# Kernel tuning notes

Measured on AMD Instinct MI355X. Metric: run time of the kernel, lower is better.

Reference implementation:

```python
import jax, jax.numpy as jnp
import numpy as np

DIM = 384
NH = 12
HEAD = DIM // NH
WS = (7, 7, 7)
L = WS[0] * WS[1] * WS[2]          # 343 tokens per window
NW = 64                             # number of windows (mask.shape[0])
B = 1                               # batch per window group
N = B * NW                          # leading dim of x
TBL = (2 * WS[0] - 1) * (2 * WS[1] - 1) * (2 * WS[2] - 1)  # 2197
SCALE = HEAD ** -0.5


def _rel_index():
    # Standard Swin 3D relative position index, shape (L, L), values in [0, TBL)
    coords = np.stack(np.meshgrid(*[np.arange(w) for w in WS], indexing='ij')).reshape(3, -1)  # (3, L)
    rel = coords[:, :, None] - coords[:, None, :]                     # (3, L, L)
    rel = rel + (np.array(WS) - 1)[:, None, None]                     # shift to >= 0
    s1 = (2 * WS[1] - 1) * (2 * WS[2] - 1)
    s2 = (2 * WS[2] - 1)
    idx = rel[0] * s1 + rel[1] * s2 + rel[2]
    return jnp.asarray(idx, jnp.int32)


def setup_inputs() -> dict:
    key = jax.random.key(0)
    k_x, k_m, k_qkv, k_tbl, k_pw = jax.random.split(key, 5)
    x = jax.random.normal(k_x, (N, L, DIM), dtype=jnp.float32)
    mask = jax.random.bernoulli(k_m, 0.5, (NW, L, L))                 # bool, True = masked
    qkv_w = jax.random.normal(k_qkv, (DIM, 3 * DIM), dtype=jnp.float32) * 0.02
    table = jax.random.normal(k_tbl, (TBL, NH), dtype=jnp.float32) * 0.02
    proj_w = jax.random.normal(k_pw, (DIM, DIM), dtype=jnp.float32) * 0.02
    proj_b = jnp.zeros((DIM,), dtype=jnp.float32)
    rel_idx = _rel_index()
    return {"x": x, "qkv_w": qkv_w, "table": table, "proj_w": proj_w,
            "proj_b": proj_b, "mask": mask, "rel_idx": rel_idx}


def reference(x, qkv_w, table, proj_w, proj_b, mask, rel_idx):
    n, l, _ = x.shape
    # QKV projection (no bias, qkv_bias=False)
    qkv = (x @ qkv_w).reshape(n, l, 3, NH, HEAD).transpose(2, 0, 3, 1, 4)  # (3, n, nh, l, ch)
    q, k, v = qkv[0], qkv[1], qkv[2]
    attn = jnp.einsum('nhlc,nhmc->nhlm', q * SCALE, k)                 # (n, nh, l, l)
    # gather relative position bias: (L*L, nh) -> (nh, L, L)
    bias = table[rel_idx.reshape(-1)].reshape(l, l, NH).transpose(2, 0, 1)
    attn = attn + bias[None]
    # per-window boolean mask: attn viewed as (batch, nw, nh, l, l)
    attn = attn.reshape(-1, NW, NH, l, l)
    attn = jnp.where(mask[None, :, None], -jnp.inf, attn).reshape(n, NH, l, l)
    attn = jax.nn.softmax(attn, axis=-1)
    out = jnp.einsum('nhlm,nhmc->nhlc', attn, v)                       # (n, nh, l, ch)
    out = out.transpose(0, 2, 1, 3).reshape(n, l, DIM)
    return out @ proj_w + proj_b
```

## Files before the change

### kernel.cpp

```cpp
#include <hip/hip_runtime.h>


#define DIMD 384
#define NHH 12
#define HEADD 32
#define LL 343
#define NWW 64
#define NTOK (NWW * LL)
#define MPT 176
#define MP (MPT * 128)
#define LP 352
#define QT 22
#define KS 40
#define VTS 360
#define PSB 40
#define MW 12
#define CSS 136
#define SCALE_ 0.17677669529663687f
#define LOG2E_ 1.4426950408889634f
#define NEGBIG_ (-1.0e4f)

typedef _Float16 f16;
typedef _Float16 v8h __attribute__((ext_vector_type(8)));
typedef _Float16 v4h __attribute__((ext_vector_type(4)));
typedef float v4f __attribute__((ext_vector_type(4)));

__device__ __forceinline__ void async_cp16(const void* g, void* l) {
    __builtin_amdgcn_global_load_lds(
        (const __attribute__((address_space(1))) void*)g,
        (__attribute__((address_space(3))) void*)l, 16, 0, 0);
}

constexpr size_t HBUF = (size_t)NHH * MP * HEADD * 2;
constexpr size_t OFF_Q    = 0;
constexpr size_t OFF_K    = OFF_Q  + HBUF;
constexpr size_t OFF_V    = OFF_K  + HBUF;
constexpr size_t OFF_AO   = OFF_V  + HBUF;
constexpr size_t OFF_BT   = OFF_AO + (size_t)MP * DIMD * 2;
constexpr size_t OFF_WT   = OFF_BT + (size_t)NHH * LP * LP * 4;
constexpr size_t OFF_PWT  = OFF_WT + (size_t)3 * DIMD * DIMD * 2;
constexpr size_t OFF_MTB  = OFF_PWT + (size_t)DIMD * DIMD * 2;

constexpr int SMEM_ATTN = LP * KS * 2 + 32 * VTS * 2 + LP * MW * 4 + 8 * 16 * PSB * 2;

#define S0 (NTOK * DIMD / 4)
#define S1 (3 * DIMD * DIMD)
#define S2 (DIMD * DIMD)
#define S3 (NHH * LP * LP)
#define S4 (NWW * MW * LP)
#define SPREP (S0 + S1 + S2 + S3 + S4)

__global__ __launch_bounds__(256) void prep_all(
    const float* __restrict__ x, f16* __restrict__ xh,
    const float* __restrict__ qkv_w, f16* __restrict__ wt,
    const float* __restrict__ proj_w, f16* __restrict__ pwt,
    const float* __restrict__ table, const int* __restrict__ rel, float* __restrict__ btf,
    const int* __restrict__ mask, unsigned int* __restrict__ mtb) {
    int t = blockIdx.x * 256 + threadIdx.x;
    if (t < S0) {
        float4 v = *(const float4*)(x + (size_t)t * 4);
        v4h o; o[0] = (f16)v.x; o[1] = (f16)v.y; o[2] = (f16)v.z; o[3] = (f16)v.w;
        *(v4h*)(xh + (size_t)t * 4) = o;
    } else if (t < S0 + S1) {
        int e = t - S0;
        int n = e / DIMD, k = e % DIMD;
        wt[e] = (f16)qkv_w[(size_t)k * (3 * DIMD) + n];
    } else if (t < S0 + S1 + S2) {
        int e = t - S0 - S1;
        int n = e / DIMD, k = e % DIMD;
        pwt[e] = (f16)proj_w[(size_t)k * DIMD + n];
    } else if (t < S0 + S1 + S2 + S3) {
        int e = t - S0 - S1 - S2;
        int h = e / (LP * LP), rem = e % (LP * LP);
        int rq = rem / (LP * 4);
        int rem2 = rem % (LP * 4);
        int col = rem2 >> 2, e2 = rem2 & 3;
        int r = rq * 4 + e2;
        float v = NEGBIG_;
        if (col < LL && r < LL) v = table[(size_t)rel[r * LL + col] * NHH + h] * LOG2E_;
        btf[e] = v;
    } else if (t < SPREP) {
        int e = t - S0 - S1 - S2 - S3;
        int n = e / (MW * LP), rem = e % (MW * LP);
        int wg = rem / LP, col = rem % LP;
        unsigned int wd = 0;
        if (col < LL) {
            int rbase = wg * 32;
#pragma unroll 4
            for (int b = 0; b < 32; ++b) {
                int r = rbase + b;
                if (r < LL && mask[((size_t)n * LL + r) * LL + col]) wd |= (1u << b);
            }
        }
        mtb[((size_t)n * LP + col) * MW + wg] = wd;
    }
}

__global__ __launch_bounds__(256) void qkv_gemm(
    const f16* __restrict__ xh, const f16* __restrict__ wt,
    f16* __restrict__ qb, f16* __restrict__ kb, f16* __restrict__ vb) {
    __shared__ f16 ABs[8192];
    f16* As = ABs;
    f16* Bs = ABs + 4096;
    const int lin = blockIdx.x;
    const int m0 = ((lin / 72) * 8 + (lin & 7)) * 128;
    const int n0 = ((lin >> 3) % 9) * 128;
    const int tid = threadIdx.x;
    const int wave = tid >> 6, lane = tid & 63;
    const int quad = lane >> 4, l15 = lane & 15;
    const int wm = (wave >> 1) * 64, wn = (wave & 1) * 64;
    const int srow = (lane >> 2);
    const int scol = (lane & 3) * 8;
    const f16* ga0 = xh + (size_t)(m0 + wave * 32 + srow) * DIMD + scol;
    const f16* ga1 = xh + (size_t)(m0 + wave * 32 + 16 + srow) * DIMD + scol;
    const f16* gb0 = wt + (size_t)(n0 + wave * 32 + srow) * DIMD + scol;
    const f16* gb1 = wt + (size_t)(n0 + wave * 32 + 16 + srow) * DIMD + scol;
    f16* la0 = As + (wave * 2) * 512;
    f16* la1 = As + (wave * 2 + 1) * 512;
    f16* lb0 = Bs + (wave * 2) * 512;
    f16* lb1 = Bs + (wave * 2 + 1) * 512;
    v4f acc[4][4] = {};
    for (int k0 = 0; k0 < DIMD; k0 += 32) {
        async_cp16(ga0 + k0, la0);
        async_cp16(ga1 + k0, la1);
        async_cp16(gb0 + k0, lb0);
        async_cp16(gb1 + k0, lb1);
        __syncthreads();
        v8h a[4], b[4];
#pragma unroll
        for (int i = 0; i < 4; ++i) a[i] = *(const v8h*)(As + (wm + i * 16 + l15) * 32 + quad * 8);
#pragma unroll
        for (int j = 0; j < 4; ++j) b[j] = *(const v8h*)(Bs + (wn + j * 16 + l15) * 32 + quad * 8);
#pragma unroll
        for (int i = 0; i < 4; ++i)
#pragma unroll
            for (int j = 0; j < 4; ++j)
                acc[i][j] = __builtin_amdgcn_mfma_f32_16x16x32_f16(a[i], b[j], acc[i][j], 0, 0, 0);
        __syncthreads();
    }
    const int t = n0 / DIMD;
    f16* dst = (t == 0) ? qb : (t == 1) ? kb : vb;
    const float sc = (t == 0) ? (SCALE_ * LOG2E_) : 1.0f;
    const int nrel = n0 - t * DIMD;
    f16* Cs = ABs;
    const int rl0 = (wave >> 1) * 16 + quad * 4;
#pragma unroll
    for (int i = 0; i < 4; ++i) {
#pragma unroll
        for (int e = 0; e < 4; ++e)
#pragma unroll
            for (int j = 0; j < 4; ++j)
                Cs[(rl0 + e) * CSS + wn + j * 16 + l15] = (f16)(acc[i][j][e] * sc);
        __syncthreads();
#pragma unroll
        for (int c = 0; c < 2; ++c) {
            int idx = c * 256 + tid;
            int rl = idx >> 4, col8 = (idx & 15) * 8;
            int gm = m0 + ((rl < 16) ? (i * 16 + rl) : (48 + i * 16 + rl));
            if (gm < NTOK) {
                int col = nrel + col8;
                size_t off = (size_t)(col >> 5) * ((size_t)MP * HEADD)
                           + (col & 31) + (size_t)gm * HEADD;
                *(v8h*)(dst + off) = *(const v8h*)(Cs + rl * CSS + col8);
            }
        }
        __syncthreads();
    }
}

__global__ __launch_bounds__(512, 4) void attn_kernel(
    const f16* __restrict__ qb, const f16* __restrict__ kb, const f16* __restrict__ vb,
    const float* __restrict__ biasT, const unsigned int* __restrict__ mtb,
    f16* __restrict__ ao) {
    extern __shared__ char smem[];
    f16* Ks  = (f16*)smem;
    f16* Vts = Ks + LP * KS;
    unsigned int* mtbL = (unsigned int*)(Vts + 32 * VTS);
    f16* Ps  = (f16*)(mtbL + LP * MW);
    const int n = blockIdx.x, h = blockIdx.y;
    const int tid = threadIdx.x, wave = tid >> 6, lane = tid & 63;
    const int quad = lane >> 4, l15 = lane & 15;
    const size_t slice = ((size_t)h * MP + n * LL) * HEADD;
    const f16* qg = qb + slice;
    const f16* kg = kb + slice;
    const f16* vg = vb + slice;
    for (int i = tid; i < LL * 8; i += 512) {
        int row = i >> 3, c4 = i & 7;
        *(ushort4*)(Ks + row * KS + c4 * 4) = *(const ushort4*)(kg + i * 4);
    }
    for (int i = tid; i < (LP - LL) * 8; i += 512) {
        int row = LL + (i >> 3), c4 = i & 7;
        *(ushort4*)(Ks + row * KS + c4 * 4) = make_ushort4(0, 0, 0, 0);
    }
    for (int i = tid; i < LL * 8; i += 512) {
        int key = i >> 3, c4 = (i & 7) * 4;
        ushort4 vv = *(const ushort4*)(vg + key * HEADD + c4);
        f16* d = Vts + c4 * VTS + key;
        d[0] = *(const f16*)&vv.x; d[VTS] = *(const f16*)&vv.y;
        d[2 * VTS] = *(const f16*)&vv.z; d[3 * VTS] = *(const f16*)&vv.w;
    }
    for (int i = tid; i < 32 * (LP - LL); i += 512) {
        int ch = i / (LP - LL), key = LL + i % (LP - LL);
        Vts[ch * VTS + key] = (f16)0.f;
    }
    {
        const unsigned int* mg = mtb + (size_t)n * LP * MW;
        for (int i = tid; i < LP * MW; i += 512) mtbL[i] = mg[i];
    }
    __syncthreads();
    f16* Pw = Ps + wave * (16 * PSB);
    const float* bth = biasT + (size_t)h * LP * LP;
    const v8h ones = {(f16)1.f, (f16)1.f, (f16)1.f, (f16)1.f,
                      (f16)1.f, (f16)1.f, (f16)1.f, (f16)1.f};
    for (int qt = wave; qt < QT; qt += 8) {
        v8h af = *(const v8h*)(qg + (qt * 16 + l15) * HEADD + quad * 8);
        const int r0 = qt * 16 + quad * 4;
        const int rword = r0 >> 5, rsh = r0 & 31;
        const float* bq = bth + (size_t)(qt * 4 + quad) * (LP * 4);
        v4f o0 = {}, o1 = {}, o2 = {};
        v4f cinN[2];
        cinN[0] = *(const v4f*)(bq + (size_t)l15 * 4);
        cinN[1] = *(const v4f*)(bq + (size_t)(16 + l15) * 4);
#pragma unroll
        for (int ktp = 0; ktp < 11; ++ktp) {
            v4f cin[2] = {cinN[0], cinN[1]};
            if (ktp < 10) {
                cinN[0] = *(const v4f*)(bq + (size_t)((ktp * 2 + 2) * 16 + l15) * 4);
                cinN[1] = *(const v4f*)(bq + (size_t)((ktp * 2 + 3) * 16 + l15) * 4);
            }
            unsigned int mw[2]; v8h bf[2]; v4f s[2];
#pragma unroll
            for (int half = 0; half < 2; ++half) {
                const int col = (ktp * 2 + half) * 16 + l15;
                mw[half] = mtbL[col * MW + rword];
                bf[half] = *(const v8h*)(Ks + col * KS + quad * 8);
            }
#pragma unroll
            for (int half = 0; half < 2; ++half) {
                v4f c = cin[half];
#pragma unroll
                for (int e = 0; e < 4; ++e)
                    if ((mw[half] >> (rsh + e)) & 1u) c[e] = NEGBIG_;
                s[half] = __builtin_amdgcn_mfma_f32_16x16x32_f16(af, bf[half], c, 0, 0, 0);
            }
#pragma unroll
            for (int half = 0; half < 2; ++half)
#pragma unroll
                for (int e = 0; e < 4; ++e) {
                    float p = __builtin_amdgcn_exp2f(s[half][e]);
                    Pw[(quad * 4 + e) * PSB + half * 16 + l15] = (f16)p;
                }
            v8h a  = *(const v8h*)(Pw + l15 * PSB + quad * 8);
            v8h b0 = *(const v8h*)(Vts + l15 * VTS + ktp * 32 + quad * 8);
            v8h b1 = *(const v8h*)(Vts + (16 + l15) * VTS + ktp * 32 + quad * 8);
            o0 = __builtin_amdgcn_mfma_f32_16x16x32_f16(a, b0, o0, 0, 0, 0);
            o1 = __builtin_amdgcn_mfma_f32_16x16x32_f16(a, b1, o1, 0, 0, 0);
            o2 = __builtin_amdgcn_mfma_f32_16x16x32_f16(a, ones, o2, 0, 0, 0);
        }
#pragma unroll
        for (int e = 0; e < 4; ++e) {
            int r = r0 + e;
            if (r < LL) {
                float inv = 1.f / o2[e];
                f16* orow = ao + ((size_t)(n * LL + r)) * DIMD + h * HEADD;
                orow[l15] = (f16)(o0[e] * inv);
                orow[16 + l15] = (f16)(o1[e] * inv);
            }
        }
    }
}

__global__ __launch_bounds__(256) void proj_gemm(
    const f16* __restrict__ ao, const f16* __restrict__ pwt,
    const float* __restrict__ pb, float* __restrict__ out) {
    __shared__ f16 As[128 * 32];
    __shared__ f16 Bs[128 * 32];
    const int lin = blockIdx.x;
    const int m0 = ((lin / 24) * 8 + (lin & 7)) * 128;
    const int n0 = ((lin >> 3) % 3) * 128;
    const int tid = threadIdx.x;
    const int wave = tid >> 6, lane = tid & 63;
    const int quad = lane >> 4, l15 = lane & 15;
    const int wm = (wave >> 1) * 64, wn = (wave & 1) * 64;
    const int srow = (lane >> 2);
    const int scol = (lane & 3) * 8;
    const f16* ga0 = ao + (size_t)(m0 + wave * 32 + srow) * DIMD + scol;
    const f16* ga1 = ao + (size_t)(m0 + wave * 32 + 16 + srow) * DIMD + scol;
    const f16* gb0 = pwt + (size_t)(n0 + wave * 32 + srow) * DIMD + scol;
    const f16* gb1 = pwt + (size_t)(n0 + wave * 32 + 16 + srow) * DIMD + scol;
    f16* la0 = As + (wave * 2) * 512;
    f16* la1 = As + (wave * 2 + 1) * 512;
    f16* lb0 = Bs + (wave * 2) * 512;
    f16* lb1 = Bs + (wave * 2 + 1) * 512;
    v4f acc[4][4] = {};
    for (int k0 = 0; k0 < DIMD; k0 += 32) {
        async_cp16(ga0 + k0, la0);
        async_cp16(ga1 + k0, la1);
        async_cp16(gb0 + k0, lb0);
        async_cp16(gb1 + k0, lb1);
        __syncthreads();
        v8h a[4], b[4];
#pragma unroll
        for (int i = 0; i < 4; ++i) a[i] = *(const v8h*)(As + (wm + i * 16 + l15) * 32 + quad * 8);
#pragma unroll
        for (int j = 0; j < 4; ++j) b[j] = *(const v8h*)(Bs + (wn + j * 16 + l15) * 32 + quad * 8);
#pragma unroll
        for (int i = 0; i < 4; ++i)
#pragma unroll
            for (int j = 0; j < 4; ++j)
                acc[i][j] = __builtin_amdgcn_mfma_f32_16x16x32_f16(a[i], b[j], acc[i][j], 0, 0, 0);
        __syncthreads();
    }
#pragma unroll
    for (int i = 0; i < 4; ++i)
#pragma unroll
        for (int e = 0; e < 4; ++e) {
            int gm = m0 + wm + i * 16 + quad * 4 + e;
            if (gm < NTOK) {
#pragma unroll
                for (int j = 0; j < 4; ++j) {
                    int gn = n0 + wn + j * 16 + l15;
                    out[(size_t)gm * DIMD + gn] = acc[i][j][e] + pb[gn];
                }
            }
        }
}

extern "C" void kernel_launch(void* const* d_in, const int* in_sizes, int n_in,
                              void* d_out, int out_size, void* d_ws, size_t ws_size,
                              hipStream_t stream) {
    const float* x      = (const float*)d_in[0];
    const float* qkv_w  = (const float*)d_in[1];
    const float* table  = (const float*)d_in[2];
    const float* proj_w = (const float*)d_in[3];
    const float* proj_b = (const float*)d_in[4];
    const int* mask     = (const int*)d_in[5];
    const int* rel      = (const int*)d_in[6];
    float* out = (float*)d_out;
    char* ws = (char*)d_ws;

    f16* q    = (f16*)(ws + OFF_Q);
    f16* k    = (f16*)(ws + OFF_K);
    f16* v    = (f16*)(ws + OFF_V);
    f16* xh   = (f16*)(ws + OFF_AO);
    f16* ao   = (f16*)(ws + OFF_AO);
    float* bt = (float*)(ws + OFF_BT);
    f16* wt   = (f16*)(ws + OFF_WT);
    f16* pwt  = (f16*)(ws + OFF_PWT);
    unsigned int* mtb = (unsigned int*)(ws + OFF_MTB);

    hipFuncSetAttribute((const void*)attn_kernel,
                        hipFuncAttributeMaxDynamicSharedMemorySize, SMEM_ATTN);

    prep_all<<<(SPREP + 255) / 256, 256, 0, stream>>>(
        x, xh, qkv_w, wt, proj_w, pwt, table, rel, bt, mask, mtb);
    qkv_gemm<<<dim3(MPT * 9), 256, 0, stream>>>(xh, wt, q, k, v);
    attn_kernel<<<dim3(NWW, NHH), 512, SMEM_ATTN, stream>>>(q, k, v, bt, mtb, ao);
    proj_gemm<<<dim3(MPT * 3), 256, 0, stream>>>(ao, pwt, proj_b, out);
}
```

Before: 227.0 us.

## Shrink attention LDS: reuse K padding for P staging, read mask from global

The attention kernel drops its separate LDS buffers for the mask bits and the per-wave P tile. P is now staged in the unused padding columns (32..39) of the K rows, and mask words are prefetched from global memory into registers alongside the bias. Blocks shrink from 512 to 256 threads (4 waves, each handling more query tiles) to cut LDS use and allow more resident blocks per CU. The risks are extra global/L2 traffic for the mask and less parallelism per block, while the layout of P in the K padding looks likely to cause LDS bank conflicts.

```diff
diff --git a/kernel.cpp b/kernel.cpp
--- a/kernel.cpp
+++ b/kernel.cpp
@@ -13,7 +13,6 @@
 #define QT 22
 #define KS 40
 #define VTS 360
-#define PSB 40
 #define MW 12
 #define CSS 136
 #define SCALE_ 0.17677669529663687f
@@ -41,7 +40,7 @@
 constexpr size_t OFF_PWT  = OFF_WT + (size_t)3 * DIMD * DIMD * 2;
 constexpr size_t OFF_MTB  = OFF_PWT + (size_t)DIMD * DIMD * 2;
 
-constexpr int SMEM_ATTN = LP * KS * 2 + 32 * VTS * 2 + LP * MW * 4 + 8 * 16 * PSB * 2;
+constexpr int SMEM_ATTN = LP * KS * 2 + 32 * VTS * 2;
 
 #define S0 (NTOK * DIMD / 4)
 #define S1 (3 * DIMD * DIMD)
@@ -168,15 +167,13 @@
     }
 }
 
-__global__ __launch_bounds__(512, 4) void attn_kernel(
+__global__ __launch_bounds__(256, 3) void attn_kernel(
     const f16* __restrict__ qb, const f16* __restrict__ kb, const f16* __restrict__ vb,
     const float* __restrict__ biasT, const unsigned int* __restrict__ mtb,
     f16* __restrict__ ao) {
     extern __shared__ char smem[];
     f16* Ks  = (f16*)smem;
     f16* Vts = Ks + LP * KS;
-    unsigned int* mtbL = (unsigned int*)(Vts + 32 * VTS);
-    f16* Ps  = (f16*)(mtbL + LP * MW);
     const int n = blockIdx.x, h = blockIdx.y;
     const int tid = threadIdx.x, wave = tid >> 6, lane = tid & 63;
     const int quad = lane >> 4, l15 = lane & 15;
@@ -184,57 +181,57 @@
     const f16* qg = qb + slice;
     const f16* kg = kb + slice;
     const f16* vg = vb + slice;
-    for (int i = tid; i < LL * 8; i += 512) {
+    for (int i = tid; i < LL * 8; i += 256) {
         int row = i >> 3, c4 = i & 7;
         *(ushort4*)(Ks + row * KS + c4 * 4) = *(const ushort4*)(kg + i * 4);
     }
-    for (int i = tid; i < (LP - LL) * 8; i += 512) {
+    for (int i = tid; i < (LP - LL) * 8; i += 256) {
         int row = LL + (i >> 3), c4 = i & 7;
         *(ushort4*)(Ks + row * KS + c4 * 4) = make_ushort4(0, 0, 0, 0);
     }
-    for (int i = tid; i < LL * 8; i += 512) {
+    for (int i = tid; i < LL * 8; i += 256) {
         int key = i >> 3, c4 = (i & 7) * 4;
         ushort4 vv = *(const ushort4*)(vg + key * HEADD + c4);
         f16* d = Vts + c4 * VTS + key;
         d[0] = *(const f16*)&vv.x; d[VTS] = *(const f16*)&vv.y;
         d[2 * VTS] = *(const f16*)&vv.z; d[3 * VTS] = *(const f16*)&vv.w;
     }
-    for (int i = tid; i < 32 * (LP - LL); i += 512) {
+    for (int i = tid; i < 32 * (LP - LL); i += 256) {
         int ch = i / (LP - LL), key = LL + i % (LP - LL);
         Vts[ch * VTS + key] = (f16)0.f;
     }
-    {
-        const unsigned int* mg = mtb + (size_t)n * LP * MW;
-        for (int i = tid; i < LP * MW; i += 512) mtbL[i] = mg[i];
-    }
     __syncthreads();
-    f16* Pw = Ps + wave * (16 * PSB);
+    f16* Pbase = Ks + (size_t)(wave * 64) * KS + 32;
+    const unsigned int* mwin = mtb + (size_t)n * LP * MW;
     const float* bth = biasT + (size_t)h * LP * LP;
     const v8h ones = {(f16)1.f, (f16)1.f, (f16)1.f, (f16)1.f,
                       (f16)1.f, (f16)1.f, (f16)1.f, (f16)1.f};
-    for (int qt = wave; qt < QT; qt += 8) {
+    for (int qt = wave; qt < QT; qt += 4) {
         v8h af = *(const v8h*)(qg + (qt * 16 + l15) * HEADD + quad * 8);
         const int r0 = qt * 16 + quad * 4;
         const int rword = r0 >> 5, rsh = r0 & 31;
         const float* bq = bth + (size_t)(qt * 4 + quad) * (LP * 4);
         v4f o0 = {}, o1 = {}, o2 = {};
-        v4f cinN[2];
+        v4f cinN[2]; unsigned int mwN[2];
         cinN[0] = *(const v4f*)(bq + (size_t)l15 * 4);
         cinN[1] = *(const v4f*)(bq + (size_t)(16 + l15) * 4);
+        mwN[0] = mwin[l15 * MW + rword];
+        mwN[1] = mwin[(16 + l15) * MW + rword];
 #pragma unroll
         for (int ktp = 0; ktp < 11; ++ktp) {
             v4f cin[2] = {cinN[0], cinN[1]};
+            unsigned int mw[2] = {mwN[0], mwN[1]};
             if (ktp < 10) {
-                cinN[0] = *(const v4f*)(bq + (size_t)((ktp * 2 + 2) * 16 + l15) * 4);
-                cinN[1] = *(const v4f*)(bq + (size_t)((ktp * 2 + 3) * 16 + l15) * 4);
-            }
-            unsigned int mw[2]; v8h bf[2]; v4f s[2];
-#pragma unroll
-            for (int half = 0; half < 2; ++half) {
-                const int col = (ktp * 2 + half) * 16 + l15;
-                mw[half] = mtbL[col * MW + rword];
-                bf[half] = *(const v8h*)(Ks + col * KS + quad * 8);
-            }
+                int c0 = (ktp * 2 + 2) * 16 + l15;
+                cinN[0] = *(const v4f*)(bq + (size_t)c0 * 4);
+                cinN[1] = *(const v4f*)(bq + (size_t)(c0 + 16) * 4);
+                mwN[0] = mwin[c0 * MW + rword];
+                mwN[1] = mwin[(c0 + 16) * MW + rword];
+            }
+            v8h bf[2]; v4f s[2];
+#pragma unroll
+            for (int half = 0; half < 2; ++half)
+                bf[half] = *(const v8h*)(Ks + ((ktp * 2 + half) * 16 + l15) * KS + quad * 8);
 #pragma unroll
             for (int half = 0; half < 2; ++half) {
                 v4f c = cin[half];
@@ -248,9 +245,9 @@
 #pragma unroll
                 for (int e = 0; e < 4; ++e) {
                     float p = __builtin_amdgcn_exp2f(s[half][e]);
-                    Pw[(quad * 4 + e) * PSB + half * 16 + l15] = (f16)p;
+                    Pbase[((quad * 4 + e) * 4 + half * 2 + (l15 >> 3)) * KS + (l15 & 7)] = (f16)p;
                 }
-            v8h a  = *(const v8h*)(Pw + l15 * PSB + quad * 8);
+            v8h a  = *(const v8h*)(Pbase + (l15 * 4 + quad) * KS);
             v8h b0 = *(const v8h*)(Vts + l15 * VTS + ktp * 32 + quad * 8);
             v8h b1 = *(const v8h*)(Vts + (16 + l15) * VTS + ktp * 32 + quad * 8);
             o0 = __builtin_amdgcn_mfma_f32_16x16x32_f16(a, b0, o0, 0, 0, 0);
@@ -355,6 +352,6 @@
     prep_all<<<(SPREP + 255) / 256, 256, 0, stream>>>(
         x, xh, qkv_w, wt, proj_w, pwt, table, rel, bt, mask, mtb);
     qkv_gemm<<<dim3(MPT * 9), 256, 0, stream>>>(xh, wt, q, k, v);
-    attn_kernel<<<dim3(NWW, NHH), 512, SMEM_ATTN, stream>>>(q, k, v, bt, mtb, ao);
+    attn_kernel<<<dim3(NWW, NHH), 256, SMEM_ATTN, stream>>>(q, k, v, bt, mtb, ao);
     proj_gemm<<<dim3(MPT * 3), 256, 0, stream>>>(ao, pwt, proj_b, out);
 }
```

After: 236.6 us. 1.04x slower.
